# Kernel tuning notes

Measured on AMD Instinct MI355X. Metric: run time of the kernel, lower is better.

The kernel has to match this reference:

```python
import jax, jax.numpy as jnp
import numpy as np

B, S, E = 2, 2048, 2048
H = 16
KV_RANK = 512
ROPE = 64
NOPE = 64  # source sets qk_nope_dim = qk_rope_dim
VD = 128   # v_head_dim = head_dim
QD = ROPE + NOPE  # q_head_dim = 128


def setup_inputs() -> dict:
    key = jax.random.key(0)
    ks = jax.random.split(key, 5)
    sd = lambda fan_in: 1.0 / np.sqrt(fan_in)
    return {
        "x": jax.random.normal(ks[0], (B, S, E), jnp.float32),
        "attention_mask": jnp.zeros((1, 1, S, S), jnp.float32),
        "W_kv_down": jax.random.normal(ks[1], (KV_RANK + ROPE, E), jnp.float32) * sd(E),
        "W_kv_up": jax.random.normal(ks[2], (H * (VD + NOPE), KV_RANK), jnp.float32) * sd(KV_RANK),
        "W_q": jax.random.normal(ks[3], (H * QD, E), jnp.float32) * sd(E),
        "W_out": jax.random.normal(ks[4], (E, H * VD), jnp.float32) * sd(H * VD),
    }


def reference(x, attention_mask, W_kv_down, W_kv_up, W_q, W_out):
    scale = QD ** (-0.5)
    # down-project to latent + rope part
    compressed = jnp.einsum('bse,fe->bsf', x, W_kv_down)          # [B,S,KV_RANK+ROPE]
    kv_c, k_rope = compressed[..., :KV_RANK], compressed[..., KV_RANK:]
    # up-project latent to per-head v and k_nope
    kv_exp = jnp.einsum('bsr,fr->bsf', kv_c, W_kv_up)             # [B,S,H*(VD+NOPE)]
    kv_exp = kv_exp.reshape(B, S, H, VD + NOPE).transpose(0, 2, 1, 3)  # [B,H,S,VD+NOPE]
    v, k_nope = kv_exp[..., :VD], kv_exp[..., VD:]
    # shared rope key broadcast over heads, concat [rope, nope]
    k_rope_b = jnp.broadcast_to(k_rope[:, None], (B, H, S, ROPE))
    k = jnp.concatenate([k_rope_b, k_nope], axis=-1)              # [B,H,S,QD]
    # queries
    q = jnp.einsum('bse,fe->bsf', x, W_q).reshape(B, S, H, QD).transpose(0, 2, 1, 3)
    scores = jnp.einsum('bhsd,bhtd->bhst', q, k) * scale + attention_mask
    w = jax.nn.softmax(scores, axis=-1)
    out = jnp.einsum('bhst,bhtv->bhsv', w, v)                     # [B,H,S,VD]
    out = out.transpose(0, 2, 1, 3).reshape(B, S, H * VD)
    return jnp.einsum('bsf,ef->bse', out, W_out)
```

## Files before the change

kernel.cpp:

```cpp
#include <hip/hip_runtime.h>
#include <hip/hip_bf16.h>
#include <stdint.h>

typedef __bf16 bf16x8 __attribute__((ext_vector_type(8)));
typedef float f32x4 __attribute__((ext_vector_type(4)));
typedef unsigned short ushort_t;

#define MFMA16 __builtin_amdgcn_mfma_f32_16x16x32_bf16

static constexpr int Bc = 2, Sc = 2048, Ec = 2048, Hc = 16;

__device__ __forceinline__ void gload16(const void* g, void* l) {
  __builtin_amdgcn_global_load_lds(
      (const __attribute__((address_space(1))) void*)g,
      (__attribute__((address_space(3))) void*)l, 16, 0, 0);
}

__device__ __forceinline__ ushort_t f2bf(float f) {
  uint32_t u = __float_as_uint(f);
  uint32_t r = (u + 0x7fffu + ((u >> 16) & 1u)) >> 16;
  return (ushort_t)r;
}
__device__ __forceinline__ float bf2f(ushort_t u) {
  return __uint_as_float((uint32_t)u << 16);
}

__global__ void cast_all(const float* __restrict__ x, const float* __restrict__ Wq,
                         const float* __restrict__ Wkvu, const float* __restrict__ Wout,
                         const float* __restrict__ Wkvd,
                         ushort_t* __restrict__ xb, ushort_t* __restrict__ wq,
                         ushort_t* __restrict__ wkvu, ushort_t* __restrict__ wout,
                         ushort_t* __restrict__ wkvd) {
  int i = blockIdx.x * 256 + threadIdx.x;
  const float* src;
  ushort_t* dst;
  int j;
  if (i < 2097152) { src = x; dst = xb; j = i; }
  else if (i < 3145728) { src = Wq; dst = wq; j = i - 2097152; }
  else if (i < 3538944) { src = Wkvu; dst = wkvu; j = i - 3145728; }
  else if (i < 4587520) { src = Wout; dst = wout; j = i - 3538944; }
  else {
    j = i - 4587520;
    int row = j >> 9, col4 = j & 511;
    ushort4 o;
    if (row < 576) {
      float4 v = ((const float4*)Wkvd)[row * 512 + col4];
      o.x = f2bf(v.x); o.y = f2bf(v.y); o.z = f2bf(v.z); o.w = f2bf(v.w);
    } else { o.x = 0; o.y = 0; o.z = 0; o.w = 0; }
    ((ushort4*)wkvd)[j] = o;
    return;
  }
  float4 v = ((const float4*)src)[j];
  ushort4 o;
  o.x = f2bf(v.x); o.y = f2bf(v.y); o.z = f2bf(v.z); o.w = f2bf(v.w);
  ((ushort4*)dst)[j] = o;
}

__global__ void mask_rearrange(const float* __restrict__ mask, ushort_t* __restrict__ m2) {
  const float INVLN2 = 1.4426950408889634f;
  int i = blockIdx.x * 256 + threadIdx.x;
  if (i >= 2048 * 32 * 16) return;
  int q = i >> 9, rest = i & 511, kb = rest >> 4, l16 = rest & 15;
  const float* src = mask + (size_t)q * 2048 + kb * 64 + l16;
  ushort4 o;
  o.x = f2bf(src[0] * INVLN2); o.y = f2bf(src[16] * INVLN2);
  o.z = f2bf(src[32] * INVLN2); o.w = f2bf(src[48] * INVLN2);
  ((ushort4*)m2)[i] = o;
}

template<int MODE>
__global__ __launch_bounds__(256, 2)
void gemm_bt(const ushort_t* __restrict__ A, int lda,
             const ushort_t* __restrict__ Bm, int ldb,
             void* __restrict__ Cout, int ldc,
             int M, int N, int K,
             char* __restrict__ vtb, char* __restrict__ kbuf)
{
  __shared__ __align__(16) ushort_t sA[128 * 32];
  __shared__ __align__(16) ushort_t sB[128 * 32];
  int tid = threadIdx.x;
  int nTn = N >> 7;
  int bid = blockIdx.x;
  int chunk = gridDim.x >> 3;
  bid = (bid & 7) * chunk + (bid >> 3);
  int tm = bid / nTn, tn = bid - tm * nTn;
  int wave = tid >> 6, lane = tid & 63;
  int wm = (wave >> 1) << 6, wn = (wave & 1) << 6;
  int l16 = lane & 15, g16 = lane >> 4;
  f32x4 acc[4][4] = {};
  int srow = tid >> 2, scol = (tid & 3) << 3;
  const ushort_t* Ag = A + (size_t)(tm * 128 + srow) * lda + scol;
  const ushort_t* Bg = Bm + (size_t)(tn * 128 + srow) * ldb + scol;
  ushort_t* sAp = &sA[srow * 32 + scol];
  ushort_t* sBp = &sB[srow * 32 + scol];
  for (int kt = 0; kt < K; kt += 32) {
    gload16(Ag, sAp);
    gload16(Ag + (size_t)64 * lda, sAp + 64 * 32);
    gload16(Bg, sBp);
    gload16(Bg + (size_t)64 * ldb, sBp + 64 * 32);
    Ag += 32; Bg += 32;
    __syncthreads();
    bf16x8 af[4], bfr[4];
#pragma unroll
    for (int i = 0; i < 4; i++) af[i] = *(const bf16x8*)&sA[(wm + i * 16 + l16) * 32 + g16 * 8];
#pragma unroll
    for (int i = 0; i < 4; i++) bfr[i] = *(const bf16x8*)&sB[(wn + i * 16 + l16) * 32 + g16 * 8];
#pragma unroll
    for (int i = 0; i < 4; i++)
#pragma unroll
      for (int j = 0; j < 4; j++)
        acc[i][j] = MFMA16(af[i], bfr[j], acc[i][j], 0, 0, 0);
    __syncthreads();
  }
#pragma unroll
  for (int i = 0; i < 4; i++) {
#pragma unroll
    for (int j = 0; j < 4; j++) {
#pragma unroll
      for (int r = 0; r < 4; r++) {
        int grow = tm * 128 + wm + i * 16 + g16 * 4 + r;
        int gcol = tn * 128 + wn + j * 16 + l16;
        float v = acc[i][j][r];
        if constexpr (MODE == 0) {
          ((ushort_t*)Cout)[(size_t)grow * ldc + gcol] = f2bf(v);
        } else if constexpr (MODE == 2) {
          ((float*)Cout)[(size_t)grow * ldc + gcol] = v;
        } else {
          int h = gcol / 192, jj = gcol - h * 192;
          int b = grow >> 11, s = grow & 2047;
          size_t bh = (size_t)(b * Hc + h);
          if (jj < 128) {
            *(ushort_t*)(vtb + bh * 524288 + (size_t)jj * 4096 + ((s >> 6) * 128) +
                         ((2 * (s & 63)) ^ ((jj & 7) << 4))) = f2bf(v);
          } else {
            int col = 64 + (jj - 128);
            *(ushort_t*)(kbuf + (bh * Sc + s) * 256 + ((2 * col) ^ ((s & 7) << 4))) = f2bf(v);
          }
        }
      }
    }
  }
}

__global__ void rope_fill(const ushort_t* __restrict__ comp, char* __restrict__ kbuf) {
  int i = blockIdx.x * 256 + threadIdx.x;
  if (i >= Bc * Sc * 8) return;
  int blk = i & 7;
  int m = i >> 3;
  int s = m & 2047, b = m >> 11;
  uint4 v = *(const uint4*)&comp[(size_t)m * 640 + 512 + blk * 8];
  int off = (blk * 16) ^ ((s & 7) << 4);
#pragma unroll
  for (int h = 0; h < Hc; h++) {
    *(uint4*)(kbuf + ((size_t)(b * Hc + h) * Sc + s) * 256 + off) = v;
  }
}

__global__ __launch_bounds__(256, 4)
void attn_kernel(const ushort_t* __restrict__ qb, const char* __restrict__ kbuf,
                 const char* __restrict__ vtb, const ushort_t* __restrict__ m2,
                 ushort_t* __restrict__ attn_o)
{
  __shared__ __align__(16) char smem[40960];
  char* sK = smem;
  char* sV = smem + 16384;
  char* sP = smem + 32768;
  const float scale2 = 0.12752081738040466f;
  int bid = blockIdx.x;
  bid = (bid & 7) * 128 + (bid >> 3);
  int qt = bid & 31, bh = bid >> 5;
  int b = bh >> 4, h = bh & 15;
  int tid = threadIdx.x, wave = tid >> 6, lane = tid & 63;
  int l16 = lane & 15, g16 = lane >> 4;

  bf16x8 qf[4];
  {
    int qrow = qt * 64 + wave * 16 + l16;
    const ushort_t* qp = qb + (size_t)(b * Sc + qrow) * 2048 + h * 128 + g16 * 8;
#pragma unroll
    for (int kf = 0; kf < 4; kf++) qf[kf] = *(const bf16x8*)(qp + kf * 32);
  }

  float mrun[4], lrun[4];
#pragma unroll
  for (int r = 0; r < 4; r++) { mrun[r] = -3.0e38f; lrun[r] = 0.f; }
  f32x4 acco[8] = {};

  const char* kg = kbuf + (size_t)bh * Sc * 256;
  const char* vg = vtb + (size_t)bh * 524288;
  char* pB = sP + wave * 2048;

  for (int kt = 0; kt < 32; kt++) {
#pragma unroll
    for (int it = 0; it < 4; it++)
      gload16(kg + kt * 16384 + it * 4096 + tid * 16, sK + it * 4096 + tid * 16);
#pragma unroll
    for (int it = 0; it < 4; it++) {
      int l = it * 4096 + tid * 16;
      gload16(vg + (size_t)(l >> 7) * 4096 + kt * 128 + (l & 127), sV + l);
    }
    __syncthreads();

    f32x4 sc[4] = {};
    __builtin_amdgcn_s_setprio(1);
#pragma unroll
    for (int ni = 0; ni < 4; ni++) {
#pragma unroll
      for (int kf = 0; kf < 4; kf++) {
        bf16x8 kfr = *(const bf16x8*)(sK + (ni * 16 + l16) * 256 +
                                      ((kf * 64 + g16 * 16) ^ ((l16 & 7) << 4)));
        sc[ni] = MFMA16(qf[kf], kfr, sc[ni], 0, 0, 0);
      }
    }
    __builtin_amdgcn_s_setprio(0);

#pragma unroll
    for (int r = 0; r < 4; r++) {
      int q = qt * 64 + wave * 16 + g16 * 4 + r;
      ushort4 mv = ((const ushort4*)m2)[(q * 32 + kt) * 16 + l16];
      sc[0][r] = sc[0][r] * scale2 + bf2f(mv.x);
      sc[1][r] = sc[1][r] * scale2 + bf2f(mv.y);
      sc[2][r] = sc[2][r] * scale2 + bf2f(mv.z);
      sc[3][r] = sc[3][r] * scale2 + bf2f(mv.w);
    }
    float mx[4];
#pragma unroll
    for (int r = 0; r < 4; r++) {
      float m0 = fmaxf(fmaxf(sc[0][r], sc[1][r]), fmaxf(sc[2][r], sc[3][r]));
#pragma unroll
      for (int m = 1; m < 16; m <<= 1) m0 = fmaxf(m0, __shfl_xor(m0, m));
      mx[r] = m0;
    }
    bool ok = true;
#pragma unroll
    for (int r = 0; r < 4; r++) ok &= (mx[r] <= mrun[r] + 11.0f);
    if (!__all(ok)) {
#pragma unroll
      for (int r = 0; r < 4; r++) {
        float mnew = fmaxf(mrun[r], mx[r]);
        float corr = __builtin_amdgcn_exp2f(mrun[r] - mnew);
        lrun[r] *= corr;
        mrun[r] = mnew;
#pragma unroll
        for (int ni = 0; ni < 8; ni++) acco[ni][r] *= corr;
      }
    }
#pragma unroll
    for (int r = 0; r < 4; r++) {
      int rowl = g16 * 4 + r;
      char* pb = pB + rowl * 128;
      int sx = (rowl & 7) << 4;
      float rs = 0.f;
#pragma unroll
      for (int ni = 0; ni < 4; ni++) {
        float p = __builtin_amdgcn_exp2f(sc[ni][r] - mrun[r]);
        rs += p;
        *(ushort_t*)(pb + ((2 * (ni * 16 + l16)) ^ sx)) = f2bf(p);
      }
      lrun[r] += rs;
    }

    __builtin_amdgcn_s_setprio(1);
#pragma unroll
    for (int kf = 0; kf < 2; kf++) {
      bf16x8 pa = *(const bf16x8*)(pB + l16 * 128 +
                                   ((kf * 64 + g16 * 16) ^ ((l16 & 7) << 4)));
#pragma unroll
      for (int ni = 0; ni < 8; ni++) {
        bf16x8 vf = *(const bf16x8*)(sV + (ni * 16 + l16) * 128 +
                                     ((kf * 64 + g16 * 16) ^ ((l16 & 7) << 4)));
        acco[ni] = MFMA16(pa, vf, acco[ni], 0, 0, 0);
      }
    }
    __builtin_amdgcn_s_setprio(0);

    __syncthreads();
  }

#pragma unroll
  for (int r = 0; r < 4; r++) {
#pragma unroll
    for (int m = 1; m < 16; m <<= 1) lrun[r] += __shfl_xor(lrun[r], m);
  }
#pragma unroll
  for (int ni = 0; ni < 8; ni++) {
#pragma unroll
    for (int r = 0; r < 4; r++) {
      int qrow = qt * 64 + wave * 16 + g16 * 4 + r;
      int col = ni * 16 + l16;
      float o = acco[ni][r] / lrun[r];
      attn_o[(size_t)(b * Sc + qrow) * 2048 + h * 128 + col] = f2bf(o);
    }
  }
}

extern "C" void kernel_launch(void* const* d_in, const int* in_sizes, int n_in,
                              void* d_out, int out_size, void* d_ws, size_t ws_size,
                              hipStream_t stream) {
  const float* x    = (const float*)d_in[0];
  const float* mask = (const float*)d_in[1];
  const float* Wkvd = (const float*)d_in[2];
  const float* Wkvu = (const float*)d_in[3];
  const float* Wq   = (const float*)d_in[4];
  const float* Wout = (const float*)d_in[5];

  char* ws = (char*)d_ws;
  size_t off = 0;
  auto alloc = [&](size_t bytes) { char* p = ws + off; off += (bytes + 255) & ~(size_t)255; return p; };
  ushort_t* xb   = (ushort_t*)alloc((size_t)4096 * 2048 * 2);
  ushort_t* wkvd = (ushort_t*)alloc((size_t)640 * 2048 * 2);
  ushort_t* wq   = (ushort_t*)alloc((size_t)2048 * 2048 * 2);
  ushort_t* wkvu = (ushort_t*)alloc((size_t)3072 * 512 * 2);
  ushort_t* wout = (ushort_t*)alloc((size_t)2048 * 2048 * 2);
  ushort_t* comp = (ushort_t*)alloc((size_t)4096 * 640 * 2);
  ushort_t* qbuf = (ushort_t*)alloc((size_t)4096 * 2048 * 2);
  char*     kbuf = alloc((size_t)Bc * Hc * Sc * 256);
  char*     vtb  = alloc((size_t)Bc * Hc * 524288);
  ushort_t* attn_o = xb;
  ushort_t* m2 = wq;

  cast_all<<<19200, 256, 0, stream>>>(x, Wq, Wkvu, Wout, Wkvd, xb, wq, wkvu, wout, wkvd);

  gemm_bt<0><<<32 * 5, 256, 0, stream>>>(xb, 2048, wkvd, 2048, comp, 640, 4096, 640, 2048, nullptr, nullptr);
  gemm_bt<0><<<32 * 16, 256, 0, stream>>>(xb, 2048, wq, 2048, qbuf, 2048, 4096, 2048, 2048, nullptr, nullptr);
  mask_rearrange<<<4096, 256, 0, stream>>>(mask, m2);
  gemm_bt<1><<<32 * 24, 256, 0, stream>>>(comp, 640, wkvu, 512, nullptr, 0, 4096, 3072, 512, vtb, kbuf);
  rope_fill<<<32768 / 256, 256, 0, stream>>>(comp, kbuf);
  attn_kernel<<<1024, 256, 0, stream>>>(qbuf, kbuf, vtb, m2, attn_o);
  gemm_bt<2><<<32 * 16, 256, 0, stream>>>(attn_o, 2048, wout, 2048, d_out, 2048, 4096, 2048, 2048, nullptr, nullptr);
}
```

Baseline: 321.2 us.

## Compute transposed score tile in attention to make softmax row-local

Swaps the MFMA operands so each lane holds a single query row's scores. The row max and sum then need only two cross-lane shuffles instead of a 16-lane reduction per row. P is written as packed bf16 pairs via v_cvt_pk_bf16_f32 with 8-byte stores, and the mask is re-laid out so each lane loads 16-byte vectors issued before the barrier. The rescale of the output accumulator now needs shuffles to redistribute the correction factors, which adds some shuffle cost on that path.

```diff
diff --git a/kernel.cpp b/kernel.cpp
--- a/kernel.cpp
+++ b/kernel.cpp
@@ -5,6 +5,7 @@
 typedef __bf16 bf16x8 __attribute__((ext_vector_type(8)));
 typedef float f32x4 __attribute__((ext_vector_type(4)));
 typedef unsigned short ushort_t;
+typedef unsigned short ushort8v __attribute__((ext_vector_type(8)));
 
 #define MFMA16 __builtin_amdgcn_mfma_f32_16x16x32_bf16
 
@@ -23,6 +24,11 @@
 }
 __device__ __forceinline__ float bf2f(ushort_t u) {
   return __uint_as_float((uint32_t)u << 16);
+}
+__device__ __forceinline__ uint32_t cvtpk(float a, float b) {
+  uint32_t d;
+  asm("v_cvt_pk_bf16_f32 %0, %1, %2" : "=v"(d) : "v"(a), "v"(b));
+  return d;
 }
 
 __global__ void cast_all(const float* __restrict__ x, const float* __restrict__ Wq,
@@ -56,16 +62,20 @@
   ((ushort4*)dst)[j] = o;
 }
 
-__global__ void mask_rearrange(const float* __restrict__ mask, ushort_t* __restrict__ m2) {
+__global__ void mask_rearrange(const float* __restrict__ mask, ushort_t* __restrict__ m3) {
   const float INVLN2 = 1.4426950408889634f;
   int i = blockIdx.x * 256 + threadIdx.x;
-  if (i >= 2048 * 32 * 16) return;
-  int q = i >> 9, rest = i & 511, kb = rest >> 4, l16 = rest & 15;
-  const float* src = mask + (size_t)q * 2048 + kb * 64 + l16;
-  ushort4 o;
-  o.x = f2bf(src[0] * INVLN2); o.y = f2bf(src[16] * INVLN2);
-  o.z = f2bf(src[32] * INVLN2); o.w = f2bf(src[48] * INVLN2);
-  ((ushort4*)m2)[i] = o;
+  if (i >= 524288) return;
+  int half = i & 1, g = (i >> 1) & 3, kt = (i >> 3) & 31, q = i >> 8;
+  const float* s0 = mask + (size_t)q * 2048 + kt * 64 + half * 32 + g * 4;
+  float4 a = *(const float4*)s0;
+  float4 c = *(const float4*)(s0 + 16);
+  ushort8v o;
+  o[0] = f2bf(a.x * INVLN2); o[1] = f2bf(a.y * INVLN2);
+  o[2] = f2bf(a.z * INVLN2); o[3] = f2bf(a.w * INVLN2);
+  o[4] = f2bf(c.x * INVLN2); o[5] = f2bf(c.y * INVLN2);
+  o[6] = f2bf(c.z * INVLN2); o[7] = f2bf(c.w * INVLN2);
+  ((ushort8v*)m3)[i] = o;
 }
 
 template<int MODE>
@@ -158,7 +168,7 @@
 
 __global__ __launch_bounds__(256, 4)
 void attn_kernel(const ushort_t* __restrict__ qb, const char* __restrict__ kbuf,
-                 const char* __restrict__ vtb, const ushort_t* __restrict__ m2,
+                 const char* __restrict__ vtb, const ushort_t* __restrict__ m3,
                  ushort_t* __restrict__ attn_o)
 {
   __shared__ __align__(16) char smem[40960];
@@ -172,23 +182,23 @@
   int b = bh >> 4, h = bh & 15;
   int tid = threadIdx.x, wave = tid >> 6, lane = tid & 63;
   int l16 = lane & 15, g16 = lane >> 4;
+  int sx = (l16 & 7) << 4;
 
   bf16x8 qf[4];
+  int qrow = qt * 64 + wave * 16 + l16;
   {
-    int qrow = qt * 64 + wave * 16 + l16;
     const ushort_t* qp = qb + (size_t)(b * Sc + qrow) * 2048 + h * 128 + g16 * 8;
 #pragma unroll
     for (int kf = 0; kf < 4; kf++) qf[kf] = *(const bf16x8*)(qp + kf * 32);
   }
 
-  float mrun[4], lrun[4];
-#pragma unroll
-  for (int r = 0; r < 4; r++) { mrun[r] = -3.0e38f; lrun[r] = 0.f; }
+  float mrun = -3.0e38f, lrun = 0.f;
   f32x4 acco[8] = {};
 
   const char* kg = kbuf + (size_t)bh * Sc * 256;
   const char* vg = vtb + (size_t)bh * 524288;
-  char* pB = sP + wave * 2048;
+  char* pB = sP + wave * 2048 + l16 * 128;
+  const ushort8v* mq = (const ushort8v*)m3 + (size_t)qrow * 256 + g16 * 2;
 
   for (int kt = 0; kt < 32; kt++) {
 #pragma unroll
@@ -199,6 +209,8 @@
       int l = it * 4096 + tid * 16;
       gload16(vg + (size_t)(l >> 7) * 4096 + kt * 128 + (l & 127), sV + l);
     }
+    ushort8v mv0 = mq[kt * 8];
+    ushort8v mv1 = mq[kt * 8 + 1];
     __syncthreads();
 
     f32x4 sc[4] = {};
@@ -208,67 +220,64 @@
 #pragma unroll
       for (int kf = 0; kf < 4; kf++) {
         bf16x8 kfr = *(const bf16x8*)(sK + (ni * 16 + l16) * 256 +
-                                      ((kf * 64 + g16 * 16) ^ ((l16 & 7) << 4)));
-        sc[ni] = MFMA16(qf[kf], kfr, sc[ni], 0, 0, 0);
+                                      ((kf * 64 + g16 * 16) ^ sx));
+        sc[ni] = MFMA16(kfr, qf[kf], sc[ni], 0, 0, 0);
       }
     }
     __builtin_amdgcn_s_setprio(0);
 
 #pragma unroll
-    for (int r = 0; r < 4; r++) {
-      int q = qt * 64 + wave * 16 + g16 * 4 + r;
-      ushort4 mv = ((const ushort4*)m2)[(q * 32 + kt) * 16 + l16];
-      sc[0][r] = sc[0][r] * scale2 + bf2f(mv.x);
-      sc[1][r] = sc[1][r] * scale2 + bf2f(mv.y);
-      sc[2][r] = sc[2][r] * scale2 + bf2f(mv.z);
-      sc[3][r] = sc[3][r] * scale2 + bf2f(mv.w);
-    }
-    float mx[4];
-#pragma unroll
-    for (int r = 0; r < 4; r++) {
-      float m0 = fmaxf(fmaxf(sc[0][r], sc[1][r]), fmaxf(sc[2][r], sc[3][r]));
-#pragma unroll
-      for (int m = 1; m < 16; m <<= 1) m0 = fmaxf(m0, __shfl_xor(m0, m));
-      mx[r] = m0;
-    }
-    bool ok = true;
-#pragma unroll
-    for (int r = 0; r < 4; r++) ok &= (mx[r] <= mrun[r] + 11.0f);
-    if (!__all(ok)) {
-#pragma unroll
-      for (int r = 0; r < 4; r++) {
-        float mnew = fmaxf(mrun[r], mx[r]);
-        float corr = __builtin_amdgcn_exp2f(mrun[r] - mnew);
-        lrun[r] *= corr;
-        mrun[r] = mnew;
-#pragma unroll
-        for (int ni = 0; ni < 8; ni++) acco[ni][r] *= corr;
+    for (int ni = 0; ni < 4; ni++) {
+      const ushort8v& mv = (ni < 2) ? mv0 : mv1;
+      int base = (ni & 1) * 4;
+#pragma unroll
+      for (int r = 0; r < 4; r++)
+        sc[ni][r] = sc[ni][r] * scale2 + bf2f(mv[base + r]);
+    }
+    float mx = fmaxf(fmaxf(fmaxf(sc[0][0], sc[0][1]), fmaxf(sc[0][2], sc[0][3])),
+                     fmaxf(fmaxf(sc[1][0], sc[1][1]), fmaxf(sc[1][2], sc[1][3])));
+    mx = fmaxf(mx, fmaxf(fmaxf(fmaxf(sc[2][0], sc[2][1]), fmaxf(sc[2][2], sc[2][3])),
+                         fmaxf(fmaxf(sc[3][0], sc[3][1]), fmaxf(sc[3][2], sc[3][3]))));
+    mx = fmaxf(mx, __shfl_xor(mx, 16));
+    mx = fmaxf(mx, __shfl_xor(mx, 32));
+    if (!__all(mx <= mrun + 11.0f)) {
+      float mnew = fmaxf(mrun, mx);
+      float corr = __builtin_amdgcn_exp2f(mrun - mnew);
+      lrun *= corr;
+      mrun = mnew;
+      float cr0 = __shfl(corr, g16 * 4 + 0);
+      float cr1 = __shfl(corr, g16 * 4 + 1);
+      float cr2 = __shfl(corr, g16 * 4 + 2);
+      float cr3 = __shfl(corr, g16 * 4 + 3);
+#pragma unroll
+      for (int ni = 0; ni < 8; ni++) {
+        acco[ni][0] *= cr0; acco[ni][1] *= cr1;
+        acco[ni][2] *= cr2; acco[ni][3] *= cr3;
       }
     }
-#pragma unroll
-    for (int r = 0; r < 4; r++) {
-      int rowl = g16 * 4 + r;
-      char* pb = pB + rowl * 128;
-      int sx = (rowl & 7) << 4;
-      float rs = 0.f;
-#pragma unroll
-      for (int ni = 0; ni < 4; ni++) {
-        float p = __builtin_amdgcn_exp2f(sc[ni][r] - mrun[r]);
-        rs += p;
-        *(ushort_t*)(pb + ((2 * (ni * 16 + l16)) ^ sx)) = f2bf(p);
-      }
-      lrun[r] += rs;
-    }
+    float rs = 0.f;
+#pragma unroll
+    for (int ni = 0; ni < 4; ni++) {
+      float p0 = __builtin_amdgcn_exp2f(sc[ni][0] - mrun);
+      float p1 = __builtin_amdgcn_exp2f(sc[ni][1] - mrun);
+      float p2 = __builtin_amdgcn_exp2f(sc[ni][2] - mrun);
+      float p3 = __builtin_amdgcn_exp2f(sc[ni][3] - mrun);
+      rs += (p0 + p1) + (p2 + p3);
+      uint2 w;
+      w.x = cvtpk(p0, p1);
+      w.y = cvtpk(p2, p3);
+      *(uint2*)(pB + ((ni * 32 + g16 * 8) ^ sx)) = w;
+    }
+    lrun += rs;
 
     __builtin_amdgcn_s_setprio(1);
 #pragma unroll
     for (int kf = 0; kf < 2; kf++) {
-      bf16x8 pa = *(const bf16x8*)(pB + l16 * 128 +
-                                   ((kf * 64 + g16 * 16) ^ ((l16 & 7) << 4)));
+      bf16x8 pa = *(const bf16x8*)(pB + ((kf * 64 + g16 * 16) ^ sx));
 #pragma unroll
       for (int ni = 0; ni < 8; ni++) {
         bf16x8 vf = *(const bf16x8*)(sV + (ni * 16 + l16) * 128 +
-                                     ((kf * 64 + g16 * 16) ^ ((l16 & 7) << 4)));
+                                     ((kf * 64 + g16 * 16) ^ sx));
         acco[ni] = MFMA16(pa, vf, acco[ni], 0, 0, 0);
       }
     }
@@ -277,19 +286,19 @@
     __syncthreads();
   }
 
-#pragma unroll
-  for (int r = 0; r < 4; r++) {
-#pragma unroll
-    for (int m = 1; m < 16; m <<= 1) lrun[r] += __shfl_xor(lrun[r], m);
-  }
+  lrun += __shfl_xor(lrun, 16);
+  lrun += __shfl_xor(lrun, 32);
+  float lr[4];
+#pragma unroll
+  for (int r = 0; r < 4; r++) lr[r] = __shfl(lrun, g16 * 4 + r);
 #pragma unroll
   for (int ni = 0; ni < 8; ni++) {
 #pragma unroll
     for (int r = 0; r < 4; r++) {
-      int qrow = qt * 64 + wave * 16 + g16 * 4 + r;
+      int qr = qt * 64 + wave * 16 + g16 * 4 + r;
       int col = ni * 16 + l16;
-      float o = acco[ni][r] / lrun[r];
-      attn_o[(size_t)(b * Sc + qrow) * 2048 + h * 128 + col] = f2bf(o);
+      float o = acco[ni][r] / lr[r];
+      attn_o[(size_t)(b * Sc + qr) * 2048 + h * 128 + col] = f2bf(o);
     }
   }
 }
@@ -317,15 +326,15 @@
   char*     kbuf = alloc((size_t)Bc * Hc * Sc * 256);
   char*     vtb  = alloc((size_t)Bc * Hc * 524288);
   ushort_t* attn_o = xb;
-  ushort_t* m2 = wq;
+  ushort_t* m3 = wq;
 
   cast_all<<<19200, 256, 0, stream>>>(x, Wq, Wkvu, Wout, Wkvd, xb, wq, wkvu, wout, wkvd);
 
   gemm_bt<0><<<32 * 5, 256, 0, stream>>>(xb, 2048, wkvd, 2048, comp, 640, 4096, 640, 2048, nullptr, nullptr);
   gemm_bt<0><<<32 * 16, 256, 0, stream>>>(xb, 2048, wq, 2048, qbuf, 2048, 4096, 2048, 2048, nullptr, nullptr);
-  mask_rearrange<<<4096, 256, 0, stream>>>(mask, m2);
+  mask_rearrange<<<2048, 256, 0, stream>>>(mask, m3);
   gemm_bt<1><<<32 * 24, 256, 0, stream>>>(comp, 640, wkvu, 512, nullptr, 0, 4096, 3072, 512, vtb, kbuf);
   rope_fill<<<32768 / 256, 256, 0, stream>>>(comp, kbuf);
-  attn_kernel<<<1024, 256, 0, stream>>>(qbuf, kbuf, vtb, m2, attn_o);
+  attn_kernel<<<1024, 256, 0, stream>>>(qbuf, kbuf, vtb, m3, attn_o);
   gemm_bt<2><<<32 * 16, 256, 0, stream>>>(attn_o, 2048, wout, 2048, d_out, 2048, 4096, 2048, 2048, nullptr, nullptr);
 }
```

After: 294.2 us. 8.4% less time.
